# Kernel tuning notes

Measured on AMD Instinct MI355X. Metric: run time of the kernel, lower is better.

The kernel has to match this reference:

```python
import jax, jax.numpy as jnp
import numpy as np

CAP = 6.0
EPS = 1e-5

def _layernorm(x, g, b):
    mu = jnp.mean(x, axis=-1, keepdims=True)
    var = jnp.mean(jnp.square(x - mu), axis=-1, keepdims=True)
    return (x - mu) * jax.lax.rsqrt(var + EPS) * g + b

def setup_inputs() -> dict:
    key = jax.random.key(0)
    B, S, D, H = 4, 1024, 1024, 16
    DF = int(D * 2.0)
    ks = jax.random.split(key, 8)
    inp = {
        "x": jax.random.normal(ks[0], (B, S, D), dtype=jnp.float32),
        "mask": jnp.tril(jnp.ones((S, S), dtype=bool)),  # causal block mask
        "qkv_w": jax.random.normal(ks[1], (3 * D, D), dtype=jnp.float32) * 0.02,
        "qkv_b": jnp.zeros((3 * D,), dtype=jnp.float32),
        "out_w": jax.random.normal(ks[2], (D, D), dtype=jnp.float32) * 0.02,
        "out_b": jnp.zeros((D,), dtype=jnp.float32),
        "ln1_g": jnp.ones((D,), dtype=jnp.float32),
        "ln1_b": jnp.zeros((D,), dtype=jnp.float32),
        "ln2_g": jnp.ones((D,), dtype=jnp.float32),
        "ln2_b": jnp.zeros((D,), dtype=jnp.float32),
        "ff1_w": jax.random.normal(ks[3], (DF, D), dtype=jnp.float32) * 0.02,
        "ff1_b": jnp.zeros((DF,), dtype=jnp.float32),
        "ff2_w": jax.random.normal(ks[4], (D, DF), dtype=jnp.float32) * 0.02,
        "ff2_b": jnp.zeros((D,), dtype=jnp.float32),
    }
    return inp

def reference(x, mask, qkv_w, qkv_b, out_w, out_b, ln1_g, ln1_b, ln2_g, ln2_b,
              ff1_w, ff1_b, ff2_w, ff2_b):
    B, S, D = x.shape
    H = 16
    dh = D // H
    res = x
    h = _layernorm(x, ln1_g, ln1_b)
    qkv = h @ qkv_w.T + qkv_b                       # [B,S,3D]
    qkv = qkv.reshape(B, S, 3, H, dh).transpose(2, 0, 3, 1, 4)  # [3,B,H,S,dh]
    q, k, v = qkv[0], qkv[1], qkv[2]
    scores = jnp.einsum('bhqd,bhkd->bhqk', q, k) / jnp.sqrt(jnp.float32(dh))
    scores = CAP * jnp.tanh(scores / CAP)            # logit soft-cap score_mod
    scores = jnp.where(mask, scores, jnp.float32(-1e9))
    attn = jax.nn.softmax(scores, axis=-1)
    o = jnp.einsum('bhqk,bhkd->bhqd', attn, v)       # [B,H,S,dh]
    o = o.transpose(0, 2, 1, 3).reshape(B, S, D)
    x = res + (o @ out_w.T + out_b)
    h2 = _layernorm(x, ln2_g, ln2_b)
    ff = jax.nn.gelu(h2 @ ff1_w.T + ff1_b, approximate=False) @ ff2_w.T + ff2_b
    return x + ff
```

## Files before the change

### kernel.cpp

```cpp
#include <hip/hip_runtime.h>
#include <cmath>

#define NROWS 4096
#define DM    1024

typedef unsigned short u16;
typedef __attribute__((ext_vector_type(8))) short short8;
typedef __attribute__((ext_vector_type(4))) float floatx4;

__device__ __forceinline__ u16 f2bf(float f) {
    unsigned int u = __float_as_uint(f);
    return (u16)((u + 0x7fffu + ((u >> 16) & 1u)) >> 16);
}

__device__ __forceinline__ size_t pk_off(int row, int k, int KB) {
    const int rt = row >> 6, i = (row >> 4) & 3, lr = row & 15;
    const int kb = k >> 6, s = (k >> 5) & 1, lq = (k >> 3) & 3, j = k & 7;
    return ((((size_t)(rt * KB + kb) * 2 + s) * 4 + i) * 64 + lq * 16 + lr) * 8 + j;
}

__device__ __forceinline__ void async_copy16(const void* g, void* l) {
    __builtin_amdgcn_global_load_lds(
        (const __attribute__((address_space(1))) void*)g,
        (__attribute__((address_space(3))) void*)l, 16, 0, 0);
}

__global__ __launch_bounds__(256) void castw4_kernel(
    const float* __restrict__ s0, const float* __restrict__ s1,
    const float* __restrict__ s2, const float* __restrict__ s3,
    u16* __restrict__ d0, u16* __restrict__ d1,
    u16* __restrict__ d2, u16* __restrict__ d3)
{
    const int bid = blockIdx.x;
    const float* s; u16* d; int base, kbits, KB;
    if (bid < 3072)      { s = s0; d = d0; base = bid;        kbits = 10; KB = 16; }
    else if (bid < 4096) { s = s1; d = d1; base = bid - 3072; kbits = 10; KB = 16; }
    else if (bid < 6144) { s = s2; d = d2; base = bid - 4096; kbits = 10; KB = 16; }
    else                 { s = s3; d = d3; base = bid - 6144; kbits = 11; KB = 32; }
    const int idx = (base * 256 + threadIdx.x) * 4;
    const float4 v = *(const float4*)(s + idx);
    const int row = idx >> kbits, k = idx & ((1 << kbits) - 1);
    *(ushort4*)(d + pk_off(row, k, KB)) =
        make_ushort4(f2bf(v.x), f2bf(v.y), f2bf(v.z), f2bf(v.w));
}

__global__ __launch_bounds__(256) void ln_kernel(
    const float* __restrict__ x, const float* __restrict__ g,
    const float* __restrict__ beta, u16* __restrict__ out)
{
    const int row = blockIdx.x;
    const int t = threadIdx.x;
    const float4 v = ((const float4*)(x + (size_t)row * DM))[t];
    float s = v.x + v.y + v.z + v.w;
    #pragma unroll
    for (int off = 32; off > 0; off >>= 1) s += __shfl_xor(s, off);
    __shared__ float red[4];
    const int wid = t >> 6;
    if ((t & 63) == 0) red[wid] = s;
    __syncthreads();
    const float mean = (red[0] + red[1] + red[2] + red[3]) * (1.0f / DM);
    const float dx = v.x - mean, dy = v.y - mean, dz = v.z - mean, dw = v.w - mean;
    float ss = dx*dx + dy*dy + dz*dz + dw*dw;
    #pragma unroll
    for (int off = 32; off > 0; off >>= 1) ss += __shfl_xor(ss, off);
    __syncthreads();
    if ((t & 63) == 0) red[wid] = ss;
    __syncthreads();
    const float var = (red[0] + red[1] + red[2] + red[3]) * (1.0f / DM);
    const float rstd = rsqrtf(var + 1e-5f);
    const float4 gv = ((const float4*)g)[t];
    const float4 bv = ((const float4*)beta)[t];
    *(ushort4*)(out + pk_off(row, t * 4, 16)) = make_ushort4(
        f2bf(dx * rstd * gv.x + bv.x), f2bf(dy * rstd * gv.y + bv.y),
        f2bf(dz * rstd * gv.z + bv.z), f2bf(dw * rstd * gv.w + bv.w));
}

__device__ __forceinline__ float gelu_f(float v) {
    return 0.5f * v * (1.0f + erff(v * 0.70710678118654752f));
}

template <int ACT, int OUTMODE, int TM>
__global__ __launch_bounds__(256, TM == 128 ? 3 : 4) void gemm_pk_kernel(
    const u16* __restrict__ A, const u16* __restrict__ W,
    const float* __restrict__ bias, const float* __restrict__ res,
    void* __restrict__ Cout, u16* __restrict__ vtout, int N, int K)
{
    constexpr int MI = TM / 32;
    constexpr int SMEMB = (OUTMODE == 1) ? 34816 : 17408;
    __shared__ __align__(16) char smem[SMEMB];
    float* Cs = (float*)smem;

    const int tid = threadIdx.x;
    const int w = tid >> 6, l = tid & 63;
    const int lr = l & 15, lq = l >> 4;
    const int wm = w >> 1, wn = w & 1;

    const int fid = blockIdx.x;
    const int NB = (N >> 7) >> 3;
    const int xcd = fid & 7;
    const int kk = fid >> 3;
    constexpr int MT_BITS = (TM == 128) ? 5 : 6;
    constexpr int MT_MASK = (1 << MT_BITS) - 1;
    const int nt = xcd * NB + (kk >> MT_BITS);
    const int mt = kk & MT_MASK;
    const int m0 = mt * TM, n0 = nt * 128;
    const int KB = K >> 6;

    const int art = (TM == 128) ? (mt * 2 + wm) : mt;
    const u16* Ab = A + (size_t)art * KB * 4096 + l * 8;
    const u16* Wb = W + (size_t)(nt * 2 + wn) * KB * 4096 + l * 8;

    floatx4 acc[MI][4] = {};
    short8 a0[MI], b0[4], a1[MI], b1[4];
    #pragma unroll
    for (int i = 0; i < MI; i++) {
        const int fi = (TM == 128) ? i : (wm * 2 + i);
        a0[i] = *(const short8*)(Ab + fi * 512);
    }
    #pragma unroll
    for (int j = 0; j < 4; j++) b0[j] = *(const short8*)(Wb + j * 512);

    const int steps = K >> 5;
    for (int t = 0; t < steps; t += 2) {
        const u16* An = Ab + (size_t)(t + 1) * 2048;
        const u16* Wn = Wb + (size_t)(t + 1) * 2048;
        #pragma unroll
        for (int i = 0; i < MI; i++) {
            const int fi = (TM == 128) ? i : (wm * 2 + i);
            a1[i] = *(const short8*)(An + fi * 512);
        }
        #pragma unroll
        for (int j = 0; j < 4; j++) b1[j] = *(const short8*)(Wn + j * 512);
        #pragma unroll
        for (int i = 0; i < MI; i++)
            #pragma unroll
            for (int j = 0; j < 4; j++)
                acc[i][j] = __builtin_amdgcn_mfma_f32_16x16x32_bf16(a0[i], b0[j], acc[i][j], 0, 0, 0);
        if (t + 2 < steps) {
            const u16* An2 = Ab + (size_t)(t + 2) * 2048;
            const u16* Wn2 = Wb + (size_t)(t + 2) * 2048;
            #pragma unroll
            for (int i = 0; i < MI; i++) {
                const int fi = (TM == 128) ? i : (wm * 2 + i);
                a0[i] = *(const short8*)(An2 + fi * 512);
            }
            #pragma unroll
            for (int j = 0; j < 4; j++) b0[j] = *(const short8*)(Wn2 + j * 512);
        }
        #pragma unroll
        for (int i = 0; i < MI; i++)
            #pragma unroll
            for (int j = 0; j < 4; j++)
                acc[i][j] = __builtin_amdgcn_mfma_f32_16x16x32_bf16(a1[i], b1[j], acc[i][j], 0, 0, 0);
    }

    if (OUTMODE == 1 && n0 >= 2048) {
        short* Ts = (short*)smem;
        float bj[4];
        #pragma unroll
        for (int j = 0; j < 4; j++) bj[j] = bias[n0 + wn * 64 + j * 16 + lr];
        #pragma unroll
        for (int i = 0; i < 4; i++)
            #pragma unroll
            for (int j = 0; j < 4; j++) {
                const int vcol_l = wn * 64 + j * 16 + lr;
                const int sbase = wm * 64 + i * 16 + lq * 4;
                #pragma unroll
                for (int rp = 0; rp < 2; rp++) {
                    const unsigned pkv =
                        (unsigned)f2bf(acc[i][j][rp * 2] + bj[j]) |
                        ((unsigned)f2bf(acc[i][j][rp * 2 + 1] + bj[j]) << 16);
                    *(unsigned*)&Ts[vcol_l * 136 + sbase + rp * 2] = pkv;
                }
            }
        __syncthreads();
        const int bb = m0 >> 10, m0loc = m0 & 1023;
        const int R0 = bb * 1024 + (n0 - 2048);
        const int row = tid >> 1, p = tid & 1;
        u16* dst = vtout + (size_t)(R0 + row) * 1024 + m0loc + p * 64;
        const short* src = &Ts[row * 136 + p * 64];
        #pragma unroll
        for (int s = 0; s < 8; s++)
            *(short8*)(dst + s * 8) = *(const short8*)(src + s * 8);
        return;
    }

    #pragma unroll
    for (int i = 0; i < MI; i++) {
        __syncthreads();
        #pragma unroll
        for (int r = 0; r < 4; r++) {
            const int rl = wm * 16 + lq * 4 + r;
            #pragma unroll
            for (int j = 0; j < 4; j++)
                Cs[rl * 136 + wn * 64 + j * 16 + lr] = acc[i][j][r];
        }
        __syncthreads();
        #pragma unroll
        for (int q = 0; q < 2; q++) {
            const int s2 = tid * 2 + q;
            const int rid = s2 >> 4, c8 = s2 & 15;
            const int rr = m0 + (rid >> 4) * (TM / 2) + i * 16 + (rid & 15);
            const int col = c8 * 8;
            float vv[8];
            const float4 v0 = *(const float4*)&Cs[rid * 136 + col];
            const float4 v1 = *(const float4*)&Cs[rid * 136 + col + 4];
            const float4 ba = *(const float4*)&bias[n0 + col];
            const float4 bb4 = *(const float4*)&bias[n0 + col + 4];
            vv[0] = v0.x + ba.x;  vv[1] = v0.y + ba.y;  vv[2] = v0.z + ba.z;  vv[3] = v0.w + ba.w;
            vv[4] = v1.x + bb4.x; vv[5] = v1.y + bb4.y; vv[6] = v1.z + bb4.z; vv[7] = v1.w + bb4.w;
            if (ACT) {
                #pragma unroll
                for (int e = 0; e < 8; e++) vv[e] = gelu_f(vv[e]);
            }
            if (OUTMODE == 0) {
                const size_t o0 = (size_t)rr * N + n0 + col;
                if (res) {
                    const float4 r0 = *(const float4*)&res[o0];
                    const float4 r1 = *(const float4*)&res[o0 + 4];
                    vv[0]+=r0.x; vv[1]+=r0.y; vv[2]+=r0.z; vv[3]+=r0.w;
                    vv[4]+=r1.x; vv[5]+=r1.y; vv[6]+=r1.z; vv[7]+=r1.w;
                }
                *(float4*)((float*)Cout + o0)     = make_float4(vv[0], vv[1], vv[2], vv[3]);
                *(float4*)((float*)Cout + o0 + 4) = make_float4(vv[4], vv[5], vv[6], vv[7]);
            } else {
                short8 ov;
                #pragma unroll
                for (int e = 0; e < 8; e++) ov[e] = (short)f2bf(vv[e]);
                if (OUTMODE == 1)
                    *(short8*)((u16*)Cout + (size_t)rr * N + n0 + col) = ov;
                else
                    *(short8*)((u16*)Cout + pk_off(rr, n0 + col, N >> 6)) = ov;
            }
        }
    }
}

__global__ __launch_bounds__(256, 4) void attn_mfma_kernel(
    const u16* __restrict__ qkv,
    const u16* __restrict__ vt,
    u16* __restrict__ o)
{
    __shared__ __align__(16) short Ks[4096];
    __shared__ __align__(16) short Vs[4096];
    __shared__ __align__(16) short Ps[4][1152];

    const int qt = 15 - blockIdx.y;
    const int bh = blockIdx.x;
    const int b = bh >> 4, h = bh & 15;
    const int tid = threadIdx.x;
    const int w = tid >> 6, l = tid & 63;
    const int C = l & 15, Qd = l >> 4;

    short8 qf[2];
    {
        const u16* qp = qkv + (size_t)(b * 1024 + qt * 64 + w * 16 + C) * 3072 + h * 64 + Qd * 8;
        qf[0] = *(const short8*)qp;
        qf[1] = *(const short8*)(qp + 32);
    }

    const u16* kbase = qkv + (size_t)(b * 1024) * 3072 + 1024 + h * 64;
    const u16* vbase = vt + (size_t)(b * 16 + h) * 65536;

    float m_i = -1e30f, l_i = 0.f;
    floatx4 oacc[4] = {};

    for (int kt = 0; kt <= qt; kt++) {
        __syncthreads();
        #pragma unroll
        for (int ii = 0; ii < 4; ii++) {
            const int i = w * 4 + ii;
            if (i < 8) {
                const int mt = i >> 1, s = i & 1;
                async_copy16(kbase + (size_t)(kt * 64 + mt * 16 + C) * 3072 + s * 32 + Qd * 8,
                             &Ks[i * 512]);
            } else {
                const int j = i - 8, dt = j >> 1, s = j & 1;
                async_copy16(vbase + (size_t)(dt * 16 + C) * 1024 + kt * 64 + s * 32 + Qd * 8,
                             &Vs[j * 512]);
            }
        }
        __syncthreads();

        floatx4 sacc[4] = {};
        #pragma unroll
        for (int mt = 0; mt < 4; mt++)
            #pragma unroll
            for (int s = 0; s < 2; s++) {
                const short8 kf = *(const short8*)&Ks[((mt * 2 + s) * 64 + l) * 8];
                sacc[mt] = __builtin_amdgcn_mfma_f32_16x16x32_bf16(kf, qf[s], sacc[mt], 0, 0, 0);
            }

        float p[16];
        float tmax = -1e30f;
        const bool diag = (kt == qt);
        const int qrow = qt * 64 + w * 16 + C;
        #pragma unroll
        for (int mt = 0; mt < 4; mt++)
            #pragma unroll
            for (int r = 0; r < 4; r++) {
                const float sv = sacc[mt][r] * 0.125f;
                const float e = __expf(sv * (1.0f / 3.0f));
                float sc = 6.0f - 12.0f / (e + 1.0f);
                if (diag) {
                    const int krow = kt * 64 + mt * 16 + Qd * 4 + r;
                    if (krow > qrow) sc = -1e30f;
                }
                p[mt * 4 + r] = sc;
                tmax = fmaxf(tmax, sc);
            }
        tmax = fmaxf(tmax, __shfl_xor(tmax, 16));
        tmax = fmaxf(tmax, __shfl_xor(tmax, 32));
        const float mnew = fmaxf(m_i, tmax);
        const float alpha = __expf(m_i - mnew);
        float rs = 0.f;
        #pragma unroll
        for (int i = 0; i < 16; i++) { p[i] = __expf(p[i] - mnew); rs += p[i]; }
        rs += __shfl_xor(rs, 16);
        rs += __shfl_xor(rs, 32);
        l_i = l_i * alpha + rs;
        m_i = mnew;

        float av[4];
        #pragma unroll
        for (int r = 0; r < 4; r++) av[r] = __shfl(alpha, Qd * 4 + r);
        #pragma unroll
        for (int dt = 0; dt < 4; dt++)
            #pragma unroll
            for (int r = 0; r < 4; r++) oacc[dt][r] *= av[r];

        #pragma unroll
        for (int mt = 0; mt < 4; mt++)
            #pragma unroll
            for (int pr = 0; pr < 2; pr++) {
                const unsigned int pk =
                    (unsigned)f2bf(p[mt * 4 + pr * 2]) |
                    ((unsigned)f2bf(p[mt * 4 + pr * 2 + 1]) << 16);
                *(unsigned int*)&Ps[w][C * 72 + mt * 16 + Qd * 4 + pr * 2] = pk;
            }
        short8 pf[2];
        pf[0] = *(const short8*)&Ps[w][C * 72 + Qd * 8];
        pf[1] = *(const short8*)&Ps[w][C * 72 + 32 + Qd * 8];

        #pragma unroll
        for (int dt = 0; dt < 4; dt++)
            #pragma unroll
            for (int s = 0; s < 2; s++) {
                const short8 vf = *(const short8*)&Vs[((dt * 2 + s) * 64 + l) * 8];
                oacc[dt] = __builtin_amdgcn_mfma_f32_16x16x32_bf16(pf[s], vf, oacc[dt], 0, 0, 0);
            }
    }

    float linv[4];
    #pragma unroll
    for (int r = 0; r < 4; r++) linv[r] = 1.0f / __shfl(l_i, Qd * 4 + r);
    __syncthreads();
    #pragma unroll
    for (int dt = 0; dt < 4; dt++) {
        const int s = dt >> 1;
        const int lqp = (dt & 1) * 2 + (C >> 3);
        const int jj = C & 7;
        #pragma unroll
        for (int r = 0; r < 4; r++)
            Ks[((s * 4 + w) * 64 + lqp * 16 + Qd * 4 + r) * 8 + jj] =
                (short)f2bf(oacc[dt][r] * linv[r]);
    }
    __syncthreads();
    u16* obase = o + (size_t)((b * 16 + qt) * 16 + h) * 4096 + tid * 16;
    *(short8*)obase       = *(const short8*)&Ks[tid * 16];
    *(short8*)(obase + 8) = *(const short8*)&Ks[tid * 16 + 8];
}

extern "C" void kernel_launch(void* const* d_in, const int* in_sizes, int n_in,
                              void* d_out, int out_size, void* d_ws, size_t ws_size,
                              hipStream_t stream)
{
    (void)in_sizes; (void)n_in; (void)out_size; (void)ws_size;
    const float* x     = (const float*)d_in[0];
    const float* qkv_w = (const float*)d_in[2];
    const float* qkv_b = (const float*)d_in[3];
    const float* out_w = (const float*)d_in[4];
    const float* out_b = (const float*)d_in[5];
    const float* ln1_g = (const float*)d_in[6];
    const float* ln1_b = (const float*)d_in[7];
    const float* ln2_g = (const float*)d_in[8];
    const float* ln2_b = (const float*)d_in[9];
    const float* ff1_w = (const float*)d_in[10];
    const float* ff1_b = (const float*)d_in[11];
    const float* ff2_w = (const float*)d_in[12];
    const float* ff2_b = (const float*)d_in[13];
    float* out = (float*)d_out;

    u16* qkvbuf = (u16*)d_ws;
    u16* vtbuf  = (u16*)((char*)d_ws + 25165824);
    u16* hbuf   = (u16*)((char*)d_ws + 33554432);
    u16* obuf   = (u16*)((char*)d_ws + 41943040);
    u16* wq     = (u16*)((char*)d_ws + 50331648);
    u16* wo = wq + 3145728;
    u16* w1 = wo + 1048576;
    u16* w2 = w1 + 2097152;
    u16* ff1buf = qkvbuf;

    castw4_kernel<<<8192, 256, 0, stream>>>(qkv_w, out_w, ff1_w, ff2_w, wq, wo, w1, w2);

    ln_kernel<<<NROWS, 256, 0, stream>>>(x, ln1_g, ln1_b, hbuf);
    gemm_pk_kernel<0,1,128><<<768, 256, 0, stream>>>(
        hbuf, wq, qkv_b, nullptr, qkvbuf, vtbuf, 3072, 1024);
    attn_mfma_kernel<<<dim3(64, 16), 256, 0, stream>>>(qkvbuf, vtbuf, obuf);
    gemm_pk_kernel<0,0,64><<<512, 256, 0, stream>>>(
        obuf, wo, out_b, x, out, nullptr, 1024, 1024);
    ln_kernel<<<NROWS, 256, 0, stream>>>(out, ln2_g, ln2_b, hbuf);
    gemm_pk_kernel<1,2,128><<<512, 256, 0, stream>>>(
        hbuf, w1, ff1_b, nullptr, ff1buf, nullptr, 2048, 1024);
    gemm_pk_kernel<0,0,64><<<512, 256, 0, stream>>>(
        ff1buf, w2, ff2_b, out, out, nullptr, 1024, 2048);
}
```

Before: 321.2 us.

## Drop online-softmax max tracking using softcap bound; fuse weight cast with LN1

The attention softmax now exploits the soft-cap bound: scores lie in [-6,6], so exp(score-6) is computed directly as exp2 of a folded constant, with no running max, no rescale of the accumulators and no alpha shuffles. The tanh and exp are folded into two exp2 calls plus a hardware reciprocal, and bf16 packing uses the library conversion. Separately, the weight-cast kernel and the first layernorm are merged into one launch with extra blocks. The change relies on the fixed cap to keep exponentials in range and trades a little accuracy for the fast reciprocal.

Result: faster. 310.4 us (-3.4%).

```diff
diff --git a/kernel.cpp b/kernel.cpp
--- a/kernel.cpp
+++ b/kernel.cpp
@@ -1,4 +1,5 @@
 #include <hip/hip_runtime.h>
+#include <hip/hip_bf16.h>
 #include <cmath>
 
 #define NROWS 4096
@@ -7,6 +8,17 @@
 typedef unsigned short u16;
 typedef __attribute__((ext_vector_type(8))) short short8;
 typedef __attribute__((ext_vector_type(4))) float floatx4;
+
+#if __has_builtin(__builtin_amdgcn_exp2f)
+#define EXP2F(x) __builtin_amdgcn_exp2f(x)
+#else
+#define EXP2F(x) exp2f(x)
+#endif
+#if __has_builtin(__builtin_amdgcn_rcpf)
+#define RCPF(x) __builtin_amdgcn_rcpf(x)
+#else
+#define RCPF(x) (1.0f / (x))
+#endif
 
 __device__ __forceinline__ u16 f2bf(float f) {
     unsigned int u = __float_as_uint(f);
@@ -25,23 +37,53 @@
         (__attribute__((address_space(3))) void*)l, 16, 0, 0);
 }
 
-__global__ __launch_bounds__(256) void castw4_kernel(
+__global__ __launch_bounds__(256) void castln_kernel(
     const float* __restrict__ s0, const float* __restrict__ s1,
     const float* __restrict__ s2, const float* __restrict__ s3,
     u16* __restrict__ d0, u16* __restrict__ d1,
-    u16* __restrict__ d2, u16* __restrict__ d3)
+    u16* __restrict__ d2, u16* __restrict__ d3,
+    const float* __restrict__ x, const float* __restrict__ g,
+    const float* __restrict__ beta, u16* __restrict__ hout)
 {
     const int bid = blockIdx.x;
-    const float* s; u16* d; int base, kbits, KB;
-    if (bid < 3072)      { s = s0; d = d0; base = bid;        kbits = 10; KB = 16; }
-    else if (bid < 4096) { s = s1; d = d1; base = bid - 3072; kbits = 10; KB = 16; }
-    else if (bid < 6144) { s = s2; d = d2; base = bid - 4096; kbits = 10; KB = 16; }
-    else                 { s = s3; d = d3; base = bid - 6144; kbits = 11; KB = 32; }
-    const int idx = (base * 256 + threadIdx.x) * 4;
-    const float4 v = *(const float4*)(s + idx);
-    const int row = idx >> kbits, k = idx & ((1 << kbits) - 1);
-    *(ushort4*)(d + pk_off(row, k, KB)) =
-        make_ushort4(f2bf(v.x), f2bf(v.y), f2bf(v.z), f2bf(v.w));
+    if (bid < 8192) {
+        const float* s; u16* d; int base, kbits, KB;
+        if (bid < 3072)      { s = s0; d = d0; base = bid;        kbits = 10; KB = 16; }
+        else if (bid < 4096) { s = s1; d = d1; base = bid - 3072; kbits = 10; KB = 16; }
+        else if (bid < 6144) { s = s2; d = d2; base = bid - 4096; kbits = 10; KB = 16; }
+        else                 { s = s3; d = d3; base = bid - 6144; kbits = 11; KB = 32; }
+        const int idx = (base * 256 + threadIdx.x) * 4;
+        const float4 v = *(const float4*)(s + idx);
+        const int row = idx >> kbits, k = idx & ((1 << kbits) - 1);
+        *(ushort4*)(d + pk_off(row, k, KB)) =
+            make_ushort4(f2bf(v.x), f2bf(v.y), f2bf(v.z), f2bf(v.w));
+        return;
+    }
+    const int row = bid - 8192;
+    const int t = threadIdx.x;
+    const float4 v = ((const float4*)(x + (size_t)row * DM))[t];
+    float s = v.x + v.y + v.z + v.w;
+    #pragma unroll
+    for (int off = 32; off > 0; off >>= 1) s += __shfl_xor(s, off);
+    __shared__ float red[4];
+    const int wid = t >> 6;
+    if ((t & 63) == 0) red[wid] = s;
+    __syncthreads();
+    const float mean = (red[0] + red[1] + red[2] + red[3]) * (1.0f / DM);
+    const float dx = v.x - mean, dy = v.y - mean, dz = v.z - mean, dw = v.w - mean;
+    float ss = dx*dx + dy*dy + dz*dz + dw*dw;
+    #pragma unroll
+    for (int off = 32; off > 0; off >>= 1) ss += __shfl_xor(ss, off);
+    __syncthreads();
+    if ((t & 63) == 0) red[wid] = ss;
+    __syncthreads();
+    const float var = (red[0] + red[1] + red[2] + red[3]) * (1.0f / DM);
+    const float rstd = rsqrtf(var + 1e-5f);
+    const float4 gv = ((const float4*)g)[t];
+    const float4 bv = ((const float4*)beta)[t];
+    *(ushort4*)(hout + pk_off(row, t * 4, 16)) = make_ushort4(
+        f2bf(dx * rstd * gv.x + bv.x), f2bf(dy * rstd * gv.y + bv.y),
+        f2bf(dz * rstd * gv.z + bv.z), f2bf(dw * rstd * gv.w + bv.w));
 }
 
 __global__ __launch_bounds__(256) void ln_kernel(
@@ -252,6 +294,8 @@
     const int w = tid >> 6, l = tid & 63;
     const int C = l & 15, Qd = l >> 4;
 
+    const float C1f = 0.0601122935f, C2f = -17.3123404907f;
+
     short8 qf[2];
     {
         const u16* qp = qkv + (size_t)(b * 1024 + qt * 64 + w * 16 + C) * 3072 + h * 64 + Qd * 8;
@@ -262,7 +306,7 @@
     const u16* kbase = qkv + (size_t)(b * 1024) * 3072 + 1024 + h * 64;
     const u16* vbase = vt + (size_t)(b * 16 + h) * 65536;
 
-    float m_i = -1e30f, l_i = 0.f;
+    float l_i = 0.f;
     floatx4 oacc[4] = {};
 
     for (int kt = 0; kt <= qt; kt++) {
@@ -292,51 +336,34 @@
             }
 
         float p[16];
-        float tmax = -1e30f;
+        float rs = 0.f;
         const bool diag = (kt == qt);
         const int qrow = qt * 64 + w * 16 + C;
         #pragma unroll
         for (int mt = 0; mt < 4; mt++)
             #pragma unroll
             for (int r = 0; r < 4; r++) {
-                const float sv = sacc[mt][r] * 0.125f;
-                const float e = __expf(sv * (1.0f / 3.0f));
-                float sc = 6.0f - 12.0f / (e + 1.0f);
+                const float e = EXP2F(sacc[mt][r] * C1f);
+                float pv = EXP2F(C2f * RCPF(e + 1.0f));
                 if (diag) {
                     const int krow = kt * 64 + mt * 16 + Qd * 4 + r;
-                    if (krow > qrow) sc = -1e30f;
+                    if (krow > qrow) pv = 0.f;
                 }
-                p[mt * 4 + r] = sc;
-                tmax = fmaxf(tmax, sc);
-            }
-        tmax = fmaxf(tmax, __shfl_xor(tmax, 16));
-        tmax = fmaxf(tmax, __shfl_xor(tmax, 32));
-        const float mnew = fmaxf(m_i, tmax);
-        const float alpha = __expf(m_i - mnew);
-        float rs = 0.f;
-        #pragma unroll
-        for (int i = 0; i < 16; i++) { p[i] = __expf(p[i] - mnew); rs += p[i]; }
+                p[mt * 4 + r] = pv;
+                rs += pv;
+            }
         rs += __shfl_xor(rs, 16);
         rs += __shfl_xor(rs, 32);
-        l_i = l_i * alpha + rs;
-        m_i = mnew;
-
-        float av[4];
-        #pragma unroll
-        for (int r = 0; r < 4; r++) av[r] = __shfl(alpha, Qd * 4 + r);
-        #pragma unroll
-        for (int dt = 0; dt < 4; dt++)
-            #pragma unroll
-            for (int r = 0; r < 4; r++) oacc[dt][r] *= av[r];
+        l_i += rs;
 
         #pragma unroll
         for (int mt = 0; mt < 4; mt++)
             #pragma unroll
             for (int pr = 0; pr < 2; pr++) {
-                const unsigned int pk =
-                    (unsigned)f2bf(p[mt * 4 + pr * 2]) |
-                    ((unsigned)f2bf(p[mt * 4 + pr * 2 + 1]) << 16);
-                *(unsigned int*)&Ps[w][C * 72 + mt * 16 + Qd * 4 + pr * 2] = pk;
+                union { __hip_bfloat162 b2; unsigned u; } cv;
+                cv.b2 = __float22bfloat162_rn(
+                    make_float2(p[mt * 4 + pr * 2], p[mt * 4 + pr * 2 + 1]));
+                *(unsigned*)&Ps[w][C * 72 + mt * 16 + Qd * 4 + pr * 2] = cv.u;
             }
         short8 pf[2];
         pf[0] = *(const short8*)&Ps[w][C * 72 + Qd * 8];
@@ -353,7 +380,7 @@
 
     float linv[4];
     #pragma unroll
-    for (int r = 0; r < 4; r++) linv[r] = 1.0f / __shfl(l_i, Qd * 4 + r);
+    for (int r = 0; r < 4; r++) linv[r] = RCPF(__shfl(l_i, Qd * 4 + r));
     __syncthreads();
     #pragma unroll
     for (int dt = 0; dt < 4; dt++) {
@@ -401,9 +428,8 @@
     u16* w2 = w1 + 2097152;
     u16* ff1buf = qkvbuf;
 
-    castw4_kernel<<<8192, 256, 0, stream>>>(qkv_w, out_w, ff1_w, ff2_w, wq, wo, w1, w2);
-
-    ln_kernel<<<NROWS, 256, 0, stream>>>(x, ln1_g, ln1_b, hbuf);
+    castln_kernel<<<12288, 256, 0, stream>>>(
+        qkv_w, out_w, ff1_w, ff2_w, wq, wo, w1, w2, x, ln1_g, ln1_b, hbuf);
     gemm_pk_kernel<0,1,128><<<768, 256, 0, stream>>>(
         hbuf, wq, qkv_b, nullptr, qkvbuf, vtbuf, 3072, 1024);
     attn_mfma_kernel<<<dim3(64, 16), 256, 0, stream>>>(qkvbuf, vtbuf, obuf);
```
